# Kernel tuning notes

Measured on AMD Instinct MI355X. Metric: run time of the kernel, lower is better.

## Reference

```python
import jax, jax.numpy as jnp
import numpy as np

# Fixed by module source: forward hardcodes a 200x200 BEV grid, dim=128,
# MSDeformAttn(n_levels=1, n_heads=4, n_points=8).
B, Z, X, C, H, P = 2, 200, 200, 128, 4, 8
N = Z * X
D = C // H  # head dim = 32


def setup_inputs() -> dict:
    key = jax.random.key(0)
    ks = jax.random.split(key, 12)
    s = 0.02
    return {
        "query": jax.random.normal(ks[0], (B, N, C), jnp.float32),
        # MSDeformAttn.value_proj
        "Wv": jax.random.normal(ks[1], (C, C), jnp.float32) * s,
        "bv": jnp.zeros((C,), jnp.float32),
        # MSDeformAttn.sampling_offsets (C -> H*1*P*2)
        "Woff": jax.random.normal(ks[2], (C, H * P * 2), jnp.float32) * s,
        "boff": jax.random.normal(ks[3], (H * P * 2,), jnp.float32) * 2.0,
        # MSDeformAttn.attention_weights (C -> H*1*P)
        "Wattn": jax.random.normal(ks[4], (C, H * P), jnp.float32) * s,
        "battn": jnp.zeros((H * P,), jnp.float32),
        # MSDeformAttn.output_proj
        "Wout1": jax.random.normal(ks[5], (C, C), jnp.float32) * s,
        "bout1": jnp.zeros((C,), jnp.float32),
        # VanillaSelfAttention.output_proj
        "Wout2": jax.random.normal(ks[6], (C, C), jnp.float32) * s,
        "bout2": jnp.zeros((C,), jnp.float32),
    }


def _forward(query, Wv, bv, Woff, boff, Wattn, battn, Wout1, bout1, Wout2, bout2):
    # Reference points: normalized centers of the 200x200 grid, order (z, x).
    zc = (jnp.arange(Z, dtype=jnp.float32) + 0.5) / Z
    xc = (jnp.arange(X, dtype=jnp.float32) + 0.5) / X
    ref = jnp.stack(jnp.meshgrid(zc, xc, indexing="ij"), axis=-1).reshape(N, 2)

    # value_proj on input_flatten (== query); split heads, lay out as images.
    value = (query @ Wv + bv).reshape(B, Z, X, H, D)
    value_flat = value.transpose(0, 3, 1, 2, 4).reshape(B * H, Z * X, D)  # (BH, ZX, D)

    # Sampling locations: ref + offsets / offset_normalizer ([W, H] = [200, 200]).
    off = (query @ Woff + boff).reshape(B, N, H, P, 2)
    norm = jnp.array([X, Z], jnp.float32)
    loc = ref[None, :, None, None, :] + off / norm  # (B, N, H, P, 2)

    # Attention weights: softmax over n_levels*n_points (= P here).
    attn = jax.nn.softmax((query @ Wattn + battn).reshape(B, N, H, P), axis=-1)

    # grid_sample convention: grid = 2*loc - 1, grid[...,0]=x (width), align_corners=False.
    grid = 2.0 * loc - 1.0
    ix = ((grid[..., 0] + 1.0) * X - 1.0) * 0.5  # pixel x coords
    iy = ((grid[..., 1] + 1.0) * Z - 1.0) * 0.5  # pixel y coords
    ix = ix.transpose(0, 2, 1, 3).reshape(B * H, N * P)
    iy = iy.transpose(0, 2, 1, 3).reshape(B * H, N * P)

    x0f = jnp.floor(ix); y0f = jnp.floor(iy)
    lx = ix - x0f; ly = iy - y0f
    x0 = x0f.astype(jnp.int32); y0 = y0f.astype(jnp.int32)
    x1 = x0 + 1; y1 = y0 + 1

    def corner(xi, yi, w):
        # zero padding: out-of-bounds corners contribute 0
        valid = (xi >= 0) & (xi < X) & (yi >= 0) & (yi < Z)
        idx = jnp.clip(yi, 0, Z - 1) * X + jnp.clip(xi, 0, X - 1)  # (BH, N*P)
        v = jnp.take_along_axis(value_flat, idx[..., None], axis=1)  # (BH, N*P, D)
        return v * (w * valid.astype(w.dtype))[..., None]

    sampled = (
        corner(x0, y0, (1.0 - lx) * (1.0 - ly))
        + corner(x1, y0, lx * (1.0 - ly))
        + corner(x0, y1, (1.0 - lx) * ly)
        + corner(x1, y1, lx * ly)
    ).reshape(B, H, N, P, D)

    # Weighted reduce over points, merge heads.
    out = jnp.einsum("bhnpd,bnhp->bnhd", sampled, attn).reshape(B, N, C)
    out = out @ Wout1 + bout1  # MSDeformAttn.output_proj
    out = out @ Wout2 + bout2  # VanillaSelfAttention.output_proj
    return out + query  # dropout is identity in eval; residual add


def reference(query, Wv, bv, Woff, boff, Wattn, battn, Wout1, bout1, Wout2, bout2):
    return _forward(query, Wv, bv, Woff, boff, Wattn, battn, Wout1, bout1, Wout2, bout2)
```

## Files before the change

### kernel.cpp

```cpp
#include <hip/hip_runtime.h>
#include <hip/hip_bf16.h>
#include <cstddef>

namespace {
constexpr int B  = 2;
constexpr int Z  = 200;
constexpr int X  = 200;
constexpr int C  = 128;
constexpr int H  = 4;
constexpr int P  = 8;
constexpr int N  = Z * X;
constexpr int BN = B * N;
constexpr int SC = 128;
constexpr int NF_P = 14;
constexpr int NF_O = 8;
constexpr int KS   = 4;

typedef __attribute__((ext_vector_type(8))) short short8;
typedef __attribute__((ext_vector_type(4))) float f32x4;
typedef _Float16 h16x2 __attribute__((ext_vector_type(2)));

__device__ inline ushort f2bf(float x) {
    __hip_bfloat16 h = __float2bfloat16(x);
    return *reinterpret_cast<ushort*>(&h);
}
__device__ inline unsigned packbf(float a, float b) {
    return (unsigned)f2bf(a) | ((unsigned)f2bf(b) << 16);
}
__device__ inline ushort f2h(float x) {
    _Float16 h = (_Float16)x;
    return __builtin_bit_cast(ushort, h);
}
__device__ inline float h1f(ushort u) {
    return (float)__builtin_bit_cast(_Float16, u);
}
__device__ inline float2 h2f2(unsigned u) {
    h16x2 h = __builtin_bit_cast(h16x2, u);
    return make_float2((float)h[0], (float)h[1]);
}
__device__ inline unsigned packh(float a, float b) {
    return (unsigned)f2h(a) | ((unsigned)f2h(b) << 16);
}
__device__ inline h16x2 pkrtz(float a, float b) {
    return __builtin_bit_cast(h16x2, __builtin_amdgcn_cvt_pkrtz(a, b));
}
template <int MASK>
__device__ inline float swzx(float x) {
    constexpr int pat = (MASK << 10) | 0x1F;
    return __int_as_float(__builtin_amdgcn_ds_swizzle(__float_as_int(x), pat));
}
template <int MASK>
__device__ inline h16x2 swzh(h16x2 x) {
    constexpr int pat = (MASK << 10) | 0x1F;
    int t = __builtin_amdgcn_ds_swizzle(__builtin_bit_cast(int, x), pat);
    return __builtin_bit_cast(h16x2, t);
}
}

__global__ __launch_bounds__(256) void vsa_k_w12(
    const float* __restrict__ Wout1, const float* __restrict__ bout1,
    const float* __restrict__ Wout2, const float* __restrict__ bout2,
    float* __restrict__ w12)
{
    const int c = threadIdx.x & 127;
    const int k = blockIdx.x * 2 + (threadIdx.x >> 7);
    if (k > 128) return;
    const float* arow = (k < 128) ? (Wout1 + (size_t)k * 128) : bout1;
    float acc = (k < 128) ? 0.f : bout2[c];
    #pragma unroll 4
    for (int j = 0; j < 128; ++j)
        acc = fmaf(arow[j], Wout2[(size_t)j * 128 + c], acc);
    w12[(size_t)k * 128 + c] = acc;
}

__global__ __launch_bounds__(256) void vsa_k_prep(
    const float* __restrict__ Wv,    const float* __restrict__ bv,
    const float* __restrict__ Woff,  const float* __restrict__ boff,
    const float* __restrict__ Wattn, const float* __restrict__ battn,
    const float* __restrict__ w12,
    ushort* __restrict__ wtp, ushort* __restrict__ wtp2,
    float* __restrict__ biasp, float* __restrict__ bias2)
{
    const int u = blockIdx.x * 256 + threadIdx.x;
    constexpr int NP = KS * NF_P * 64;
    constexpr int NO = KS * NF_O * 64;

    if (u < NP) {
        int ks  = u / (NF_P * 64);
        int rem = u - ks * (NF_P * 64);
        int f = rem >> 6, l = rem & 63;
        int n  = f * 16 + (l & 15);
        int kb = ks * 32 + (l >> 4) * 8;
        float v[8];
        #pragma unroll
        for (int e = 0; e < 8; ++e) {
            int k = kb + e;
            if (n < 128)      v[e] = Wv[k * 128 + n];
            else if (n < 192) v[e] = Woff[k * 64 + (n - 128)];
            else              v[e] = Wattn[k * 32 + (n - 192)];
        }
        unsigned* dst = (unsigned*)(wtp + (size_t)u * 8);
        #pragma unroll
        for (int i = 0; i < 4; ++i) dst[i] = packbf(v[2*i], v[2*i+1]);
    } else if (u < NP + NO) {
        int t   = u - NP;
        int ks  = t / (NF_O * 64);
        int rem = t - ks * (NF_O * 64);
        int f = rem >> 6, l = rem & 63;
        int n  = f * 16 + (l & 15);
        int kb = ks * 32 + (l >> 4) * 8;
        unsigned* dst = (unsigned*)(wtp2 + (size_t)t * 8);
        #pragma unroll
        for (int i = 0; i < 4; ++i)
            dst[i] = packh(w12[(size_t)(kb + 2*i) * 128 + n],
                           w12[(size_t)(kb + 2*i + 1) * 128 + n]);
    } else if (u < NP + NO + 224) {
        int c = u - NP - NO;
        float bb;
        if (c < 128)      bb = bv[c];
        else if (c < 192) bb = boff[c - 128];
        else              bb = battn[c - 192];
        biasp[c] = bb;
    } else if (u < NP + NO + 224 + 128) {
        int c = u - NP - NO - 224;
        bias2[c] = w12[(size_t)128 * 128 + c];
    }
}

__global__ __launch_bounds__(512) void vsa_k_proj(
    const float* __restrict__ Q, const ushort* __restrict__ wtp,
    const float* __restrict__ biasp,
    ushort* __restrict__ proj_v16, ushort* __restrict__ proj_s16)
{
    __shared__ ushort lds_wt[KS * NF_P * 64 * 8];

    const int tid  = threadIdx.x;
    const int lane = tid & 63;
    const int wv   = tid >> 6;
    const int row0 = blockIdx.x * 128 + wv * 16;
    const int m  = lane & 15;
    const int kg = lane >> 4;

    {
        const uint4* src = (const uint4*)wtp;
        uint4* dst = (uint4*)lds_wt;
        #pragma unroll
        for (int it = 0; it < 7; ++it)
            dst[it * 512 + tid] = src[it * 512 + tid];
    }
    __syncthreads();

    const float* qp = Q + (size_t)(row0 + m) * 128 + kg * 8;

    f32x4 acc[NF_P];
    #pragma unroll
    for (int f = 0; f < NF_P; ++f) acc[f] = (f32x4){0.f, 0.f, 0.f, 0.f};

    #pragma unroll
    for (int ks = 0; ks < KS; ++ks) {
        float4 a0 = *(const float4*)(qp + ks * 32);
        float4 a1 = *(const float4*)(qp + ks * 32 + 4);
        short8 af;
        af[0] = (short)f2bf(a0.x); af[1] = (short)f2bf(a0.y);
        af[2] = (short)f2bf(a0.z); af[3] = (short)f2bf(a0.w);
        af[4] = (short)f2bf(a1.x); af[5] = (short)f2bf(a1.y);
        af[6] = (short)f2bf(a1.z); af[7] = (short)f2bf(a1.w);
        const short8* wrow = (const short8*)lds_wt + ks * NF_P * 64 + lane;
        #pragma unroll
        for (int f = 0; f < NF_P; ++f)
            acc[f] = __builtin_amdgcn_mfma_f32_16x16x32_bf16(af, wrow[f * 64], acc[f], 0, 0, 0);
    }

    #pragma unroll
    for (int f = 0; f < 8; ++f) {
        const int col = f * 16 + m;
        const float bb = biasp[col];
        #pragma unroll
        for (int r = 0; r < 4; ++r)
            proj_v16[(size_t)(row0 + kg * 4 + r) * 128 + col] = f2h(acc[f][r] + bb);
    }
    #pragma unroll
    for (int f = 8; f < 12; ++f) {
        const int col = f * 16 + m;
        const float bb = biasp[col];
        const int c  = col - 128;
        const int hp = c >> 1, comp = c & 1;
        #pragma unroll
        for (int r = 0; r < 4; ++r)
            proj_s16[(size_t)(row0 + kg * 4 + r) * SC + hp * 4 + comp] = f2h(acc[f][r] + bb);
    }
    #pragma unroll
    for (int f = 12; f < 14; ++f) {
        const float bb = biasp[f * 16 + m];
        const int hp = (f - 12) * 16 + m;
        #pragma unroll
        for (int r = 0; r < 4; ++r) {
            float v = acc[f][r] + bb;
            float mx = v;
            mx = fmaxf(mx, swzx<1>(mx));
            mx = fmaxf(mx, swzx<2>(mx));
            mx = fmaxf(mx, swzx<4>(mx));
            float ex = __expf(v - mx);
            float sm = ex;
            sm += swzx<1>(sm); sm += swzx<2>(sm); sm += swzx<4>(sm);
            const float wp = ex / sm;
            proj_s16[(size_t)(row0 + kg * 4 + r) * SC + hp * 4 + 2] = f2h(wp);
        }
    }
}

__global__ __launch_bounds__(1024) void vsa_k_so(
    const ushort* __restrict__ proj_v16, const ushort* __restrict__ proj_s16,
    const ushort* __restrict__ wtp2, const float* __restrict__ bias2,
    const float* __restrict__ Q, float* __restrict__ out)
{
    __shared__ ushort tmp_lds[16][136];

    const int lane = threadIdx.x & 63;
    const int wv   = threadIdx.x >> 6;
    const int hsub = lane >> 5;
    const int p    = (lane >> 2) & 7;
    const int d8   = lane & 3;

    const int orig = blockIdx.x;
    const int wg   = (orig & 7) * 625 + (orig >> 3);
    const int b    = wg / 2500;
    const int bl0  = (wg - b * 2500) * 16;
    const int i0   = bl0 / 200;
    const int j0   = bl0 - i0 * 200;
    const int bn0  = b * N + bl0;

    const ushort* vb = proj_v16 + (size_t)b * N * 128;

    #pragma unroll
    for (int t = 0; t < 2; ++t) {
        const int unit = t * 16 + wv;
        const int pix  = unit >> 1;
        const int h    = (unit & 1) * 2 + hsub;
        const int jr   = j0 + pix;
        const bool wr  = jr >= 200;
        const int i    = i0 + (wr ? 1 : 0);
        const int j    = wr ? jr - 200 : jr;
        const int bn   = bn0 + pix;

        const uint2 ow = *(const uint2*)(proj_s16 + (size_t)bn * SC + (h * 8 + p) * 4);
        const float2 off = h2f2(ow.x);
        const float  wp  = h1f((ushort)(ow.y & 0xffff));

        const float ixf = (float)i + off.x;
        const float iyf = (float)j + off.y;
        const float x0f = floorf(ixf), y0f = floorf(iyf);
        const float lx = ixf - x0f, ly = iyf - y0f;
        const int x0 = (int)x0f, y0 = (int)y0f;
        const int x1 = x0 + 1,  y1 = y0 + 1;
        const int xc0 = min(max(x0, 0), X - 1), xc1 = min(max(x1, 0), X - 1);
        const int yc0 = min(max(y0, 0), Z - 1), yc1 = min(max(y1, 0), Z - 1);

        const float wx0 = ((unsigned)x0 < (unsigned)X) ? (1.f - lx) : 0.f;
        const float wx1 = ((unsigned)x1 < (unsigned)X) ? lx : 0.f;
        const float wy0 = (((unsigned)y0 < (unsigned)Z) ? (1.f - ly) : 0.f) * wp;
        const float wy1 = (((unsigned)y1 < (unsigned)Z) ? ly : 0.f) * wp;

        const h16x2 w00p = pkrtz(wx0 * wy0, wx0 * wy0);
        const h16x2 w10p = pkrtz(wx1 * wy0, wx1 * wy0);
        const h16x2 w01p = pkrtz(wx0 * wy1, wx0 * wy1);
        const h16x2 w11p = pkrtz(wx1 * wy1, wx1 * wy1);

        const int rb0 = yc0 * X, rb1 = yc1 * X;
        const int hb  = h * 32 + d8 * 8;

        const uint4 c00 = *(const uint4*)(vb + (size_t)(rb0 + xc0) * 128 + hb);
        const uint4 c10 = *(const uint4*)(vb + (size_t)(rb0 + xc1) * 128 + hb);
        const uint4 c01 = *(const uint4*)(vb + (size_t)(rb1 + xc0) * 128 + hb);
        const uint4 c11 = *(const uint4*)(vb + (size_t)(rb1 + xc1) * 128 + hb);

        h16x2 a0 = (h16x2)0, a1 = (h16x2)0, a2 = (h16x2)0, a3 = (h16x2)0;
        #define VSA_ACC(c, wpk) { \
            a0 = __builtin_elementwise_fma(__builtin_bit_cast(h16x2, (c).x), wpk, a0); \
            a1 = __builtin_elementwise_fma(__builtin_bit_cast(h16x2, (c).y), wpk, a1); \
            a2 = __builtin_elementwise_fma(__builtin_bit_cast(h16x2, (c).z), wpk, a2); \
            a3 = __builtin_elementwise_fma(__builtin_bit_cast(h16x2, (c).w), wpk, a3); }
        VSA_ACC(c00, w00p)
        VSA_ACC(c10, w10p)
        VSA_ACC(c01, w01p)
        VSA_ACC(c11, w11p)
        #undef VSA_ACC

        a0 += swzh<4>(a0);  a1 += swzh<4>(a1);  a2 += swzh<4>(a2);  a3 += swzh<4>(a3);
        a0 += swzh<8>(a0);  a1 += swzh<8>(a1);  a2 += swzh<8>(a2);  a3 += swzh<8>(a3);
        a0 += swzh<16>(a0); a1 += swzh<16>(a1); a2 += swzh<16>(a2); a3 += swzh<16>(a3);

        if (p == 0) {
            uint4 o;
            o.x = __builtin_bit_cast(unsigned, a0);
            o.y = __builtin_bit_cast(unsigned, a1);
            o.z = __builtin_bit_cast(unsigned, a2);
            o.w = __builtin_bit_cast(unsigned, a3);
            *(uint4*)(&tmp_lds[pix][h * 32 + d8 * 8]) = o;
        }
    }

    const int m  = lane & 15;
    const int kg = lane >> 4;
    const int col = (wv & 7) * 16 + m;
    float qv[4];
    if (wv < 8) {
        #pragma unroll
        for (int r = 0; r < 4; ++r)
            qv[r] = __builtin_nontemporal_load(Q + (size_t)(bn0 + kg * 4 + r) * 128 + col);
    }

    __syncthreads();
    if (wv >= 8) return;

    f32x4 acc = (f32x4){0.f, 0.f, 0.f, 0.f};
    #pragma unroll
    for (int ks = 0; ks < KS; ++ks) {
        short8 af = *(const short8*)(&tmp_lds[m][ks * 32 + kg * 8]);
        const short8* wrow = (const short8*)wtp2 + ks * NF_O * 64 + lane;
        acc = __builtin_amdgcn_mfma_f32_16x16x32_f16(af, wrow[wv * 64], acc, 0, 0, 0);
    }

    const float bb = bias2[col];
    #pragma unroll
    for (int r = 0; r < 4; ++r) {
        const size_t gi = (size_t)(bn0 + kg * 4 + r) * 128 + col;
        __builtin_nontemporal_store(acc[r] + bb + qv[r], out + gi);
    }
}

extern "C" void kernel_launch(void* const* d_in, const int* in_sizes, int n_in,
                              void* d_out, int out_size, void* d_ws, size_t ws_size,
                              hipStream_t stream) {
    const float* Q     = (const float*)d_in[0];
    const float* Wv    = (const float*)d_in[1];
    const float* bv    = (const float*)d_in[2];
    const float* Woff  = (const float*)d_in[3];
    const float* boff  = (const float*)d_in[4];
    const float* Wattn = (const float*)d_in[5];
    const float* battn = (const float*)d_in[6];
    const float* Wout1 = (const float*)d_in[7];
    const float* bout1 = (const float*)d_in[8];
    const float* Wout2 = (const float*)d_in[9];
    const float* bout2 = (const float*)d_in[10];
    float* out = (float*)d_out;

    float*  biasp  = (float*)d_ws;
    float*  bias2  = biasp + 224;
    float*  w12    = bias2 + 128;
    ushort* proj_s16 = (ushort*)(w12 + 129 * 128);
    ushort* proj_v16 = proj_s16 + (size_t)BN * SC;
    ushort* wtp    = proj_v16 + (size_t)BN * 128;
    ushort* wtp2   = wtp + (size_t)KS * NF_P * 64 * 8;

    constexpr int prep_n = KS * NF_P * 64 + KS * NF_O * 64 + 224 + 128;
    vsa_k_w12<<<65, 256, 0, stream>>>(Wout1, bout1, Wout2, bout2, w12);
    vsa_k_prep<<<(prep_n + 255) / 256, 256, 0, stream>>>(
        Wv, bv, Woff, boff, Wattn, battn, w12, wtp, wtp2, biasp, bias2);
    vsa_k_proj<<<BN / 128, 512, 0, stream>>>(Q, wtp, biasp, proj_v16, proj_s16);
    vsa_k_so<<<BN / 16, 1024, 0, stream>>>(proj_v16, proj_s16, wtp2, bias2, Q, out);
}
```

Measured before the change: 84.99 us.

## Merge weight-prep kernels and prefetch output weights and residual before gather

The two setup kernels are combined into one launch: the Wout1·Wout2 product is written directly into the fp16 MFMA fragment layout, so the intermediate fp32 w12 buffer and the separate repack pass go away. In the sampling kernel, the offset and weight loads for both iterations are issued up front. The output-weight MFMA fragments and residual query values are also loaded into registers before the bilinear gather, so their latency overlaps with it. This removes one kernel launch and moves global loads earlier, at the cost of higher register pressure in the 1024-thread kernel.

```diff
diff --git a/kernel.cpp b/kernel.cpp
--- a/kernel.cpp
+++ b/kernel.cpp
@@ -57,34 +57,39 @@
 }
 }
 
-__global__ __launch_bounds__(256) void vsa_k_w12(
-    const float* __restrict__ Wout1, const float* __restrict__ bout1,
-    const float* __restrict__ Wout2, const float* __restrict__ bout2,
-    float* __restrict__ w12)
-{
-    const int c = threadIdx.x & 127;
-    const int k = blockIdx.x * 2 + (threadIdx.x >> 7);
-    if (k > 128) return;
-    const float* arow = (k < 128) ? (Wout1 + (size_t)k * 128) : bout1;
-    float acc = (k < 128) ? 0.f : bout2[c];
-    #pragma unroll 4
-    for (int j = 0; j < 128; ++j)
-        acc = fmaf(arow[j], Wout2[(size_t)j * 128 + c], acc);
-    w12[(size_t)k * 128 + c] = acc;
-}
-
-__global__ __launch_bounds__(256) void vsa_k_prep(
+__global__ __launch_bounds__(256) void vsa_k_setup(
     const float* __restrict__ Wv,    const float* __restrict__ bv,
     const float* __restrict__ Woff,  const float* __restrict__ boff,
     const float* __restrict__ Wattn, const float* __restrict__ battn,
-    const float* __restrict__ w12,
+    const float* __restrict__ Wout1, const float* __restrict__ bout1,
+    const float* __restrict__ Wout2, const float* __restrict__ bout2,
     ushort* __restrict__ wtp, ushort* __restrict__ wtp2,
     float* __restrict__ biasp, float* __restrict__ bias2)
 {
-    const int u = blockIdx.x * 256 + threadIdx.x;
     constexpr int NP = KS * NF_P * 64;
-    constexpr int NO = KS * NF_O * 64;
-
+
+    if (blockIdx.x < 65) {
+        const int c = threadIdx.x & 127;
+        const int k = blockIdx.x * 2 + (threadIdx.x >> 7);
+        if (k > 128) return;
+        const float* arow = (k < 128) ? (Wout1 + (size_t)k * 128) : bout1;
+        float acc = (k < 128) ? 0.f : bout2[c];
+        #pragma unroll 4
+        for (int j = 0; j < 128; ++j)
+            acc = fmaf(arow[j], Wout2[(size_t)j * 128 + c], acc);
+        if (k < 128) {
+            const int ks = k >> 5;
+            const int l  = (((k >> 3) & 3) << 4) | (c & 15);
+            const int f  = c >> 4;
+            const int t  = (ks * NF_O + f) * 64 + l;
+            wtp2[(size_t)t * 8 + (k & 7)] = f2h(acc);
+        } else {
+            bias2[c] = acc;
+        }
+        return;
+    }
+
+    const int u = (blockIdx.x - 65) * 256 + threadIdx.x;
     if (u < NP) {
         int ks  = u / (NF_P * 64);
         int rem = u - ks * (NF_P * 64);
@@ -102,28 +107,13 @@
         unsigned* dst = (unsigned*)(wtp + (size_t)u * 8);
         #pragma unroll
         for (int i = 0; i < 4; ++i) dst[i] = packbf(v[2*i], v[2*i+1]);
-    } else if (u < NP + NO) {
-        int t   = u - NP;
-        int ks  = t / (NF_O * 64);
-        int rem = t - ks * (NF_O * 64);
-        int f = rem >> 6, l = rem & 63;
-        int n  = f * 16 + (l & 15);
-        int kb = ks * 32 + (l >> 4) * 8;
-        unsigned* dst = (unsigned*)(wtp2 + (size_t)t * 8);
-        #pragma unroll
-        for (int i = 0; i < 4; ++i)
-            dst[i] = packh(w12[(size_t)(kb + 2*i) * 128 + n],
-                           w12[(size_t)(kb + 2*i + 1) * 128 + n]);
-    } else if (u < NP + NO + 224) {
-        int c = u - NP - NO;
+    } else if (u < NP + 224) {
+        int c = u - NP;
         float bb;
         if (c < 128)      bb = bv[c];
         else if (c < 192) bb = boff[c - 128];
         else              bb = battn[c - 192];
         biasp[c] = bb;
-    } else if (u < NP + NO + 224 + 128) {
-        int c = u - NP - NO - 224;
-        bias2[c] = w12[(size_t)128 * 128 + c];
     }
 }
 
@@ -231,24 +221,44 @@
     const int bn0  = b * N + bl0;
 
     const ushort* vb = proj_v16 + (size_t)b * N * 128;
-
+    const int m  = lane & 15;
+    const int kg = lane >> 4;
+    const int col = (wv & 7) * 16 + m;
+
+    int pix_t[2], h_t[2];
+    float fi_t[2], fj_t[2];
+    uint2 ow[2];
     #pragma unroll
     for (int t = 0; t < 2; ++t) {
         const int unit = t * 16 + wv;
         const int pix  = unit >> 1;
-        const int h    = (unit & 1) * 2 + hsub;
+        pix_t[t] = pix;
+        h_t[t]   = (unit & 1) * 2 + hsub;
         const int jr   = j0 + pix;
         const bool wr  = jr >= 200;
-        const int i    = i0 + (wr ? 1 : 0);
-        const int j    = wr ? jr - 200 : jr;
-        const int bn   = bn0 + pix;
-
-        const uint2 ow = *(const uint2*)(proj_s16 + (size_t)bn * SC + (h * 8 + p) * 4);
-        const float2 off = h2f2(ow.x);
-        const float  wp  = h1f((ushort)(ow.y & 0xffff));
-
-        const float ixf = (float)i + off.x;
-        const float iyf = (float)j + off.y;
+        fi_t[t] = (float)(i0 + (wr ? 1 : 0));
+        fj_t[t] = (float)(wr ? jr - 200 : jr);
+        ow[t] = *(const uint2*)(proj_s16 + (size_t)(bn0 + pix) * SC + (h_t[t] * 8 + p) * 4);
+    }
+
+    short8 wfrag[KS];
+    float qv[4];
+    if (wv < 8) {
+        #pragma unroll
+        for (int ks = 0; ks < KS; ++ks)
+            wfrag[ks] = ((const short8*)wtp2)[ks * NF_O * 64 + wv * 64 + lane];
+        #pragma unroll
+        for (int r = 0; r < 4; ++r)
+            qv[r] = __builtin_nontemporal_load(Q + (size_t)(bn0 + kg * 4 + r) * 128 + col);
+    }
+
+    #pragma unroll
+    for (int t = 0; t < 2; ++t) {
+        const float2 off = h2f2(ow[t].x);
+        const float  wp  = h1f((ushort)(ow[t].y & 0xffff));
+
+        const float ixf = fi_t[t] + off.x;
+        const float iyf = fj_t[t] + off.y;
         const float x0f = floorf(ixf), y0f = floorf(iyf);
         const float lx = ixf - x0f, ly = iyf - y0f;
         const int x0 = (int)x0f, y0 = (int)y0f;
@@ -267,7 +277,7 @@
         const h16x2 w11p = pkrtz(wx1 * wy1, wx1 * wy1);
 
         const int rb0 = yc0 * X, rb1 = yc1 * X;
-        const int hb  = h * 32 + d8 * 8;
+        const int hb  = h_t[t] * 32 + d8 * 8;
 
         const uint4 c00 = *(const uint4*)(vb + (size_t)(rb0 + xc0) * 128 + hb);
         const uint4 c10 = *(const uint4*)(vb + (size_t)(rb0 + xc1) * 128 + hb);
@@ -296,18 +306,8 @@
             o.y = __builtin_bit_cast(unsigned, a1);
             o.z = __builtin_bit_cast(unsigned, a2);
             o.w = __builtin_bit_cast(unsigned, a3);
-            *(uint4*)(&tmp_lds[pix][h * 32 + d8 * 8]) = o;
+            *(uint4*)(&tmp_lds[pix_t[t]][h_t[t] * 32 + d8 * 8]) = o;
         }
-    }
-
-    const int m  = lane & 15;
-    const int kg = lane >> 4;
-    const int col = (wv & 7) * 16 + m;
-    float qv[4];
-    if (wv < 8) {
-        #pragma unroll
-        for (int r = 0; r < 4; ++r)
-            qv[r] = __builtin_nontemporal_load(Q + (size_t)(bn0 + kg * 4 + r) * 128 + col);
     }
 
     __syncthreads();
@@ -317,8 +317,7 @@
     #pragma unroll
     for (int ks = 0; ks < KS; ++ks) {
         short8 af = *(const short8*)(&tmp_lds[m][ks * 32 + kg * 8]);
-        const short8* wrow = (const short8*)wtp2 + ks * NF_O * 64 + lane;
-        acc = __builtin_amdgcn_mfma_f32_16x16x32_f16(af, wrow[wv * 64], acc, 0, 0, 0);
+        acc = __builtin_amdgcn_mfma_f32_16x16x32_f16(af, wfrag[ks], acc, 0, 0, 0);
     }
 
     const float bb = bias2[col];
@@ -347,16 +346,16 @@
 
     float*  biasp  = (float*)d_ws;
     float*  bias2  = biasp + 224;
-    float*  w12    = bias2 + 128;
-    ushort* proj_s16 = (ushort*)(w12 + 129 * 128);
+    ushort* proj_s16 = (ushort*)(bias2 + 128);
     ushort* proj_v16 = proj_s16 + (size_t)BN * SC;
     ushort* wtp    = proj_v16 + (size_t)BN * 128;
     ushort* wtp2   = wtp + (size_t)KS * NF_P * 64 * 8;
 
-    constexpr int prep_n = KS * NF_P * 64 + KS * NF_O * 64 + 224 + 128;
-    vsa_k_w12<<<65, 256, 0, stream>>>(Wout1, bout1, Wout2, bout2, w12);
-    vsa_k_prep<<<(prep_n + 255) / 256, 256, 0, stream>>>(
-        Wv, bv, Woff, boff, Wattn, battn, w12, wtp, wtp2, biasp, bias2);
+    constexpr int NP = KS * NF_P * 64;
+    constexpr int setup_blocks = 65 + (NP + 224 + 255) / 256;
+    vsa_k_setup<<<setup_blocks, 256, 0, stream>>>(
+        Wv, bv, Woff, boff, Wattn, battn, Wout1, bout1, Wout2, bout2,
+        wtp, wtp2, biasp, bias2);
     vsa_k_proj<<<BN / 128, 512, 0, stream>>>(Q, wtp, biasp, proj_v16, proj_s16);
     vsa_k_so<<<BN / 16, 1024, 0, stream>>>(proj_v16, proj_s16, wtp2, bias2, Q, out);
 }
```

Measured after the change: 83.51 us, median of 4. Within noise of the previous version (-1.7%).
